# Kernel tuning notes

Measured on AMD Instinct MI355X. Metric: run time of the kernel, lower is better.

The kernel has to match this reference:

```python
import jax, jax.numpy as jnp
import numpy as np

HIDDEN = 2048
HEADS = 16
HEAD_DIM = HIDDEN // HEADS  # 128
MLA_DIM = max(HEAD_DIM // 4, 8)  # 32
WINDOW = 512
B, S = 4, 2048


def setup_inputs() -> dict:
    key = jax.random.key(0)
    ks = jax.random.split(key, 9)
    sc = 0.02
    return {
        "x": jax.random.normal(ks[0], (B, S, HIDDEN), jnp.float32),
        "wq": jax.random.normal(ks[1], (HIDDEN, HIDDEN), jnp.float32) * sc,
        "wk": jax.random.normal(ks[2], (HEAD_DIM, HIDDEN), jnp.float32) * sc,
        "wv": jax.random.normal(ks[3], (HEAD_DIM, HIDDEN), jnp.float32) * sc,
        "wo": jax.random.normal(ks[4], (HIDDEN, HIDDEN), jnp.float32) * sc,
        "k_compress_w": jax.random.normal(ks[5], (MLA_DIM, HEAD_DIM), jnp.float32) * sc,
        "v_compress_w": jax.random.normal(ks[6], (MLA_DIM, HEAD_DIM), jnp.float32) * sc,
        "k_decompress_w": jax.random.normal(ks[7], (HEAD_DIM, MLA_DIM), jnp.float32) * sc,
        "v_decompress_w": jax.random.normal(ks[8], (HEAD_DIM, MLA_DIM), jnp.float32) * sc,
    }


def _rope_tables(seq_len, dim):
    inv_freq = 1.0 / (10000.0 ** (jnp.arange(0, dim, 2, dtype=jnp.float32) / dim))
    t = jnp.arange(seq_len, dtype=jnp.float32)
    freqs = jnp.outer(t, inv_freq)            # [S, dim/2]
    emb = jnp.concatenate([freqs, freqs], -1)  # [S, dim]
    return jnp.cos(emb), jnp.sin(emb)


def _rotate_half(x):
    h = x.shape[-1] // 2
    return jnp.concatenate([-x[..., h:], x[..., :h]], axis=-1)


def _quant_dequant_8bit(t):
    # global min/max 8-bit fake-quant (round has zero grad, matching uint8 detach)
    t_min, t_max = t.min(), t.max()
    scale = (t_max - t_min) / 255.0
    q = jnp.clip(jnp.round((t - t_min) / scale), 0.0, 255.0)
    return q * scale + t_min


def _swat(scores):
    attn = jax.nn.sigmoid(scores)
    return attn / (attn.sum(axis=-1, keepdims=True) + 1e-8)


def reference(x, wq, wk, wv, wo, k_compress_w, v_compress_w, k_decompress_w, v_decompress_w):
    b, s, _ = x.shape
    scale = 1.0 / np.sqrt(HEAD_DIM)

    Q = (x @ wq.T).reshape(b, s, HEADS, HEAD_DIM).transpose(0, 2, 1, 3)  # [B,H,S,D]
    K = (x @ wk.T)[:, None]  # [B,1,S,D] (single shared KV head, MQA)
    V = (x @ wv.T)[:, None]

    # RoPE (cos/sin broadcast over batch and heads)
    cos, sin = _rope_tables(s, HEAD_DIM)
    Q = Q * cos + _rotate_half(Q) * sin
    K = K * cos + _rotate_half(K) * sin

    # MLA compress -> decompress (low-rank)
    K = (K @ k_compress_w.T) @ k_decompress_w.T
    V = (V @ v_compress_w.T) @ v_decompress_w.T

    # 8-bit fake quantization
    K = _quant_dequant_8bit(K)
    V = _quant_dequant_8bit(V)

    # Sliding-window SWAT attention with linear blending of overlaps
    step = WINDOW // 2
    out = jnp.zeros_like(Q)
    for i in range(0, s, step):
        e = min(i + WINDOW, s)
        Qw = Q[:, :, i:e]           # [B,H,w,D]
        Kw = K[:, :, i:e]           # [B,1,w,D]
        Vw = V[:, :, i:e]
        scores = jnp.matmul(Qw, Kw.swapaxes(-2, -1)) * scale  # [B,H,w,w]
        wout = jnp.matmul(_swat(scores), Vw)                   # [B,H,w,D]
        if i == 0:
            out = out.at[:, :, i:e].set(wout)
        else:
            ov = min(step, e - i)
            alpha = jnp.linspace(0.0, 1.0, ov).reshape(1, 1, -1, 1)
            blended = (1 - alpha) * out[:, :, i:i + ov] + alpha * wout[:, :, :ov]
            out = out.at[:, :, i:i + ov].set(blended)
            if i + ov < e:
                out = out.at[:, :, i + ov:e].set(wout[:, :, ov:])

    out = out.transpose(0, 2, 1, 3).reshape(b, s, HIDDEN)
    return out @ wo.T
```

## Files before the change

### kernel.cpp

```cpp
#include <hip/hip_runtime.h>
#include <hip/hip_bf16.h>
#include <hip/hip_fp16.h>
#include <math.h>

#define BB 4
#define SS 2048
#define HIDDEN 2048
#define NHEADS 16
#define HDIM 128
#define BSROWS (BB * SS)
#define ATT_SCALE 0.08838834764831845f

typedef __attribute__((ext_vector_type(8))) _Float16 half8v;
typedef __attribute__((ext_vector_type(4))) float f32x4;
typedef __attribute__((ext_vector_type(16))) float f32x16;

static __device__ __forceinline__ unsigned encf(float x) {
  unsigned b = __float_as_uint(x);
  return (b & 0x80000000u) ? ~b : (b | 0x80000000u);
}
static __device__ __forceinline__ float decf(unsigned k) {
  unsigned b = (k & 0x80000000u) ? (k ^ 0x80000000u) : ~k;
  return __uint_as_float(b);
}
static __device__ __forceinline__ unsigned short f2h(float f) {
  _Float16 h = (_Float16)f;
  return *(unsigned short*)&h;
}


__global__ void rope_tables_k(float* __restrict__ ct, float* __restrict__ st) {
  int t = blockIdx.x;
  int d = threadIdx.x;
  float inv = powf(10000.0f, -(float)d * (1.0f / 64.0f));
  float a = (float)t * inv;
  ct[t * 64 + d] = cosf(a);
  st[t * 64 + d] = sinf(a);
}

__global__ void build_m_k(const float* __restrict__ kc, const float* __restrict__ kdw,
                          const float* __restrict__ vc, const float* __restrict__ vdw,
                          float* __restrict__ mk, float* __restrict__ mv) {
  int a = blockIdx.x;
  int c = threadIdx.x;
  const float* cw = blockIdx.y ? vc : kc;
  const float* dw = blockIdx.y ? vdw : kdw;
  float* m = blockIdx.y ? mv : mk;
  float acc = 0.f;
#pragma unroll
  for (int mm = 0; mm < 32; mm++) acc += cw[mm * 128 + a] * dw[c * 32 + mm];
  m[a * 128 + c] = acc;
}

__global__ void mm_init_k(unsigned* mmx) {
  int i = threadIdx.x;
  if (i < 4) mmx[i] = (i & 1) ? 0u : 0xFFFFFFFFu;
}

__global__ void split_fp16_k(const float* __restrict__ src,
                             unsigned short* __restrict__ hi, int n4) {
  int i = blockIdx.x * 256 + threadIdx.x;
  int stride = gridDim.x * 256;
  for (; i < n4; i += stride) {
    float4 v = ((const float4*)src)[i];
    ((ushort4*)hi)[i] = make_ushort4(f2h(v.x), f2h(v.y), f2h(v.z), f2h(v.w));
  }
}

__global__ __launch_bounds__(512, 2) void gemm_f16_ph_k(
    const unsigned short* __restrict__ A, const unsigned short* __restrict__ B,
    float* __restrict__ Cf, unsigned short* __restrict__ Ch, int NBX) {
  __shared__ unsigned short As[2][256 * 64];
  __shared__ unsigned short Bs[2][256 * 64];
  const int K = 2048;
  const int nsteps = 32;
  int tid = threadIdx.x;
  int lane = tid & 63;
  int wid = tid >> 6;
  int wm = wid >> 2, wn = wid & 3;
  int l31 = lane & 31, lg2 = lane >> 5;
  int swz = (l31 & 7) << 4;

  int nwg = gridDim.x;
  int cpx = nwg >> 3;
  int sbid = ((int)blockIdx.x & 7) * cpx + ((int)blockIdx.x >> 3);
  int by = sbid / NBX, bx = sbid % NBX;
  int m0 = by * 256, n0 = bx * 256;

  f32x16 acc[4][2] = {};

#define STAGE_A_HALF(tt_, h_, sl_)                                                 \
  do {                                                                             \
    int k0a_ = (tt_) << 6;                                                         \
    _Pragma("unroll") for (int j_ = 0; j_ < 2; ++j_) {                             \
      int L_ = j_ * 8192 + tid * 16;                                               \
      int hr_ = L_ >> 7;                                                           \
      int r_ = (hr_ & 63) + ((hr_ & 64) << 1) + (h_) * 64;                         \
      int cb_ = (L_ & 127) ^ ((r_ & 7) << 4);                                      \
      __builtin_amdgcn_global_load_lds(                                            \
          (const __attribute__((address_space(1))) void*)(A +                      \
              (size_t)(m0 + r_) * K + k0a_ + (cb_ >> 1)),                          \
          (__attribute__((address_space(3))) void*)((char*)&As[sl_][0] +           \
              (h_) * 8192 + j_ * 16384 + tid * 16), 16, 0, 0);                     \
    }                                                                              \
  } while (0)

#define STAGE_B_HALF(tt_, h_, sl_)                                                 \
  do {                                                                             \
    int k0b_ = (tt_) << 6;                                                         \
    _Pragma("unroll") for (int j_ = 0; j_ < 2; ++j_) {                             \
      int L_ = j_ * 8192 + tid * 16;                                               \
      int hr_ = L_ >> 7;                                                           \
      int r_ = (hr_ & 63) + ((hr_ & 64) << 1) + (h_) * 64;                         \
      int cb_ = (L_ & 127) ^ ((r_ & 7) << 4);                                      \
      __builtin_amdgcn_global_load_lds(                                            \
          (const __attribute__((address_space(1))) void*)(B +                      \
              (size_t)(n0 + r_) * K + k0b_ + (cb_ >> 1)),                          \
          (__attribute__((address_space(3))) void*)((char*)&Bs[sl_][0] +           \
              (h_) * 8192 + j_ * 16384 + tid * 16), 16, 0, 0);                     \
    }                                                                              \
  } while (0)

  STAGE_A_HALF(0, 0, 0);
  STAGE_B_HALF(0, 0, 0);
  STAGE_B_HALF(0, 1, 0);
  STAGE_A_HALF(0, 1, 0);
  asm volatile("s_waitcnt vmcnt(0)" ::: "memory");
  __builtin_amdgcn_sched_barrier(0);
  __builtin_amdgcn_s_barrier();

  for (int t = 0; t < nsteps; ++t) {
    int s = t & 1;
    const char* Ab = (const char*)&As[s][0];
    const char* Bb = (const char*)&Bs[s][0];
    half8v afr[2][4], bfr[2][4];
    if (t + 1 < nsteps) {
      STAGE_A_HALF(t + 1, 0, s ^ 1);
      STAGE_B_HALF(t + 1, 0, s ^ 1);
      STAGE_B_HALF(t + 1, 1, s ^ 1);
      STAGE_A_HALF(t + 1, 1, s ^ 1);
    }
#pragma unroll
    for (int ks = 0; ks < 4; ++ks) {
      int cb = (ks * 32 + lg2 * 16) ^ swz;
      afr[0][ks] = *(const half8v*)(Ab + (wm * 128 + 0 + l31) * 128 + cb);
      afr[1][ks] = *(const half8v*)(Ab + (wm * 128 + 32 + l31) * 128 + cb);
      bfr[0][ks] = *(const half8v*)(Bb + (wn * 64 + 0 + l31) * 128 + cb);
      bfr[1][ks] = *(const half8v*)(Bb + (wn * 64 + 32 + l31) * 128 + cb);
    }
    __builtin_amdgcn_s_barrier();
    asm volatile("s_waitcnt lgkmcnt(0)" ::: "memory");
    __builtin_amdgcn_sched_barrier(0);
    __builtin_amdgcn_s_setprio(1);
#pragma unroll
    for (int ks = 0; ks < 4; ++ks) {
      acc[0][0] = __builtin_amdgcn_mfma_f32_32x32x16_f16(afr[0][ks], bfr[0][ks], acc[0][0], 0, 0, 0);
      acc[0][1] = __builtin_amdgcn_mfma_f32_32x32x16_f16(afr[0][ks], bfr[1][ks], acc[0][1], 0, 0, 0);
      acc[1][0] = __builtin_amdgcn_mfma_f32_32x32x16_f16(afr[1][ks], bfr[0][ks], acc[1][0], 0, 0, 0);
      acc[1][1] = __builtin_amdgcn_mfma_f32_32x32x16_f16(afr[1][ks], bfr[1][ks], acc[1][1], 0, 0, 0);
    }
    __builtin_amdgcn_s_setprio(0);
    if (t + 1 < nsteps)
      asm volatile("s_waitcnt vmcnt(8)" ::: "memory");
    else
      asm volatile("s_waitcnt vmcnt(0)" ::: "memory");
    __builtin_amdgcn_sched_barrier(0);
    __builtin_amdgcn_s_barrier();
#pragma unroll
    for (int ks = 0; ks < 4; ++ks) {
      int cb = (ks * 32 + lg2 * 16) ^ swz;
      afr[0][ks] = *(const half8v*)(Ab + (wm * 128 + 64 + l31) * 128 + cb);
      afr[1][ks] = *(const half8v*)(Ab + (wm * 128 + 96 + l31) * 128 + cb);
    }
    __builtin_amdgcn_s_barrier();
    asm volatile("s_waitcnt lgkmcnt(0)" ::: "memory");
    __builtin_amdgcn_sched_barrier(0);
    __builtin_amdgcn_s_setprio(1);
#pragma unroll
    for (int ks = 0; ks < 4; ++ks) {
      acc[2][0] = __builtin_amdgcn_mfma_f32_32x32x16_f16(afr[0][ks], bfr[0][ks], acc[2][0], 0, 0, 0);
      acc[2][1] = __builtin_amdgcn_mfma_f32_32x32x16_f16(afr[0][ks], bfr[1][ks], acc[2][1], 0, 0, 0);
      acc[3][0] = __builtin_amdgcn_mfma_f32_32x32x16_f16(afr[1][ks], bfr[0][ks], acc[3][0], 0, 0, 0);
      acc[3][1] = __builtin_amdgcn_mfma_f32_32x32x16_f16(afr[1][ks], bfr[1][ks], acc[3][1], 0, 0, 0);
    }
    __builtin_amdgcn_s_setprio(0);
    if (t + 1 < nsteps)
      asm volatile("s_waitcnt vmcnt(2)" ::: "memory");
    else
      asm volatile("s_waitcnt vmcnt(0)" ::: "memory");
    __builtin_amdgcn_sched_barrier(0);
    __builtin_amdgcn_s_barrier();
  }
#undef STAGE_A_HALF
#undef STAGE_B_HALF

#pragma unroll
  for (int mi = 0; mi < 4; ++mi) {
#pragma unroll
    for (int ni = 0; ni < 2; ++ni) {
      int col = n0 + wn * 64 + ni * 32 + l31;
#pragma unroll
      for (int r = 0; r < 16; ++r) {
        int row = m0 + wm * 128 + mi * 32 + (r & 3) + 8 * (r >> 2) + 4 * lg2;
        float v = acc[mi][ni][r];
        if (Ch)
          Ch[(size_t)row * 2048 + col] = f2h(v);
        else
          Cf[(size_t)row * 2048 + col] = v;
      }
    }
  }
}

__global__ __launch_bounds__(256) void gemm_f16_kv_k(
    const unsigned short* __restrict__ A, const unsigned short* __restrict__ B,
    float* __restrict__ Ckv) {
  const int K = 2048;
  __shared__ unsigned short As[128 * 64];
  __shared__ unsigned short Bs[128 * 64];
  int tid = threadIdx.x;
  int lane = tid & 63, wid = tid >> 6;
  int wr = wid >> 1, wc = wid & 1;
  int m0 = blockIdx.y * 128, n0 = blockIdx.x * 128;

  f32x4 acc[4][4] = {};

  int off_ = (wid << 10) + (lane << 4);
  int l15 = lane & 15, lk = lane >> 4;

  for (int t = 0; t < 32; ++t) {
    int k0 = t << 6;
    __syncthreads();
#pragma unroll
    for (int c = 0; c < 4; ++c) {
      int off = off_ + (c << 12);
      int row = off >> 7;
      int cole = (off & 127) >> 1;
      const unsigned short* ga = A + (size_t)(m0 + row) * K + k0 + cole;
      const unsigned short* gb = B + (size_t)(n0 + row) * K + k0 + cole;
      __builtin_amdgcn_global_load_lds(
          (const __attribute__((address_space(1))) void*)ga,
          (__attribute__((address_space(3))) void*)((char*)As + off), 16, 0, 0);
      __builtin_amdgcn_global_load_lds(
          (const __attribute__((address_space(1))) void*)gb,
          (__attribute__((address_space(3))) void*)((char*)Bs + off), 16, 0, 0);
    }
    __syncthreads();
#pragma unroll
    for (int ks = 0; ks < 2; ++ks) {
      half8v af[4], bf[4];
#pragma unroll
      for (int f = 0; f < 4; ++f) {
        int arow = wr * 64 + f * 16 + l15;
        int brow = wc * 64 + f * 16 + l15;
        int colb = ks * 64 + lk * 16;
        af[f] = *(const half8v*)((const char*)As + arow * 128 + colb);
        bf[f] = *(const half8v*)((const char*)Bs + brow * 128 + colb);
      }
#pragma unroll
      for (int fm = 0; fm < 4; ++fm)
#pragma unroll
        for (int fn = 0; fn < 4; ++fn)
          acc[fm][fn] = __builtin_amdgcn_mfma_f32_16x16x32_f16(af[fm], bf[fn], acc[fm][fn], 0, 0, 0);
    }
  }
#pragma unroll
  for (int fm = 0; fm < 4; ++fm) {
#pragma unroll
    for (int j = 0; j < 4; ++j) {
      int row = m0 + wr * 64 + fm * 16 + lk * 4 + j;
#pragma unroll
      for (int fn = 0; fn < 4; ++fn) {
        int col = n0 + wc * 64 + fn * 16 + l15;
        Ckv[(size_t)row * 256 + col] = acc[fm][fn][j];
      }
    }
  }
}

__global__ __launch_bounds__(256) void kv_transform_k(float* kvb,
                                                      const float* __restrict__ mk,
                                                      const float* __restrict__ mv,
                                                      const float* __restrict__ ct,
                                                      const float* __restrict__ st,
                                                      unsigned* mmx) {
  int which = blockIdx.y;
  float* base = kvb + which * 128;
  const float* M = which ? mv : mk;
  __shared__ float rowb[256];
  __shared__ float red[256];
  int tid = threadIdx.x;
  int half = tid >> 7, col = tid & 127;
  float vmin = 3.4e38f, vmax = -3.4e38f;
  int r0 = blockIdx.x * 64;
  for (int ri = 0; ri < 32; ri++) {
    size_t row = r0 + ri * 2 + half;
    __syncthreads();
    if (which == 0) {
      int t = (int)(row & (SS - 1));
      int j = col & 63;
      float c = ct[t * 64 + j], s = st[t * 64 + j];
      float x0 = base[row * 256 + j];
      float x1 = base[row * 256 + j + 64];
      rowb[tid] = (col < 64) ? (x0 * c - x1 * s) : (x1 * c + x0 * s);
    } else {
      rowb[tid] = base[row * 256 + col];
    }
    __syncthreads();
    float acc = 0.f;
    const float* rb = &rowb[half * 128];
#pragma unroll 8
    for (int a = 0; a < 128; a++) acc += rb[a] * M[a * 128 + col];
    base[row * 256 + col] = acc;
    vmin = fminf(vmin, acc);
    vmax = fmaxf(vmax, acc);
  }
  red[tid] = vmin;
  __syncthreads();
  for (int s2 = 128; s2 > 0; s2 >>= 1) {
    if (tid < s2) red[tid] = fminf(red[tid], red[tid + s2]);
    __syncthreads();
  }
  if (tid == 0) atomicMin(&mmx[which * 2 + 0], encf(red[0]));
  __syncthreads();
  red[tid] = vmax;
  __syncthreads();
  for (int s2 = 128; s2 > 0; s2 >>= 1) {
    if (tid < s2) red[tid] = fmaxf(red[tid], red[tid + s2]);
    __syncthreads();
  }
  if (tid == 0) atomicMax(&mmx[which * 2 + 1], encf(red[0]));
}

__global__ void quant_k_codes_k(const float* __restrict__ kvb,
                                unsigned short* __restrict__ qkc,
                                const unsigned* __restrict__ mmx) {
  int i = blockIdx.x * 256 + threadIdx.x;
  float mn = decf(mmx[0]);
  float sc = (decf(mmx[1]) - mn) * (1.f / 255.f);
  int row = i >> 7, d = i & 127;
  float v = kvb[(size_t)row * 256 + d];
  float qv = fminf(fmaxf(rintf((v - mn) / sc), 0.f), 255.f);
  qkc[i] = f2h(qv);
}

__global__ __launch_bounds__(256) void quant_vt_k(const float* __restrict__ kvb,
                                                  unsigned short* __restrict__ qvtc,
                                                  const unsigned* __restrict__ mmx) {
  int b = blockIdx.y;
  int s0 = blockIdx.x * 64;
  __shared__ unsigned short tile[128 * 72];
  float mn = decf(mmx[2]);
  float sc = (decf(mmx[3]) - mn) * (1.f / 255.f);
  for (int i = threadIdx.x; i < 8192; i += 256) {
    int sl = i >> 7, d = i & 127;
    float v = kvb[((size_t)(b * SS + s0 + sl)) * 256 + 128 + d];
    float qv = fminf(fmaxf(rintf((v - mn) / sc), 0.f), 255.f);
    tile[d * 72 + sl] = f2h(qv);
  }
  __syncthreads();
  int d = threadIdx.x >> 1, hf = threadIdx.x & 1;
  unsigned short* dst = qvtc + (size_t)(b * 128 + d) * 2048 + s0 + hf * 32;
  const unsigned short* srcp = &tile[d * 72 + hf * 32];
#pragma unroll
  for (int u = 0; u < 4; ++u)
    *(ushort4*)(dst + u * 8) = *(const ushort4*)(srcp + u * 8),
    *(ushort4*)(dst + u * 8 + 4) = *(const ushort4*)(srcp + u * 8 + 4);
}

__global__ __launch_bounds__(256, 3) void attn_mfma_k(
    const unsigned short* __restrict__ qh, const unsigned short* __restrict__ qkc,
    const unsigned short* __restrict__ qvtc, const unsigned* __restrict__ mmx,
    const float* __restrict__ ct, const float* __restrict__ st,
    unsigned short* __restrict__ outp) {
  __shared__ unsigned short Ks[64 * 128];
  __shared__ unsigned short Vt[128 * 64];
  __shared__ unsigned short Pl[64 * 64];
  int tid = threadIdx.x;
  int lane = tid & 63, w = tid >> 6;
  int l15 = lane & 15, lg = lane >> 4;
  int swk = (l15 & 7) << 4;
  int b = blockIdx.y >> 4, h = blockIdx.y & 15;
  int t0 = blockIdx.x * 64;
  int wa = t0 >> 8;

  float mnk = decf(mmx[0]), sck = (decf(mmx[1]) - mnk) * (1.f / 255.f);
  float mnv = decf(mmx[2]), scv = (decf(mmx[3]) - mnv) * (1.f / 255.f);
  float aK = ATT_SCALE * sck;
  float aMnk = ATT_SCALE * mnk;

  half8v qf[4];
  float cj[4];
  {
    int trow = t0 + w * 16 + l15;
    const unsigned short* qrow =
        qh + ((size_t)(b * SS + trow) * NHEADS + h) * HDIM + lg * 8;
    const float* cbp = ct + (size_t)trow * 64 + lg * 8;
    const float* sbp = st + (size_t)trow * 64 + lg * 8;
    float sq = 0.f;
#pragma unroll
    for (int half = 0; half < 2; ++half) {
      half8v xa8 = *(const half8v*)(qrow + half * 32);
      half8v ya8 = *(const half8v*)(qrow + half * 32 + 64);
      float4 ca = *(const float4*)(cbp + half * 32);
      float4 cb4 = *(const float4*)(cbp + half * 32 + 4);
      float4 sa = *(const float4*)(sbp + half * 32);
      float4 sb4 = *(const float4*)(sbp + half * 32 + 4);
      float cv[8] = {ca.x, ca.y, ca.z, ca.w, cb4.x, cb4.y, cb4.z, cb4.w};
      float sv[8] = {sa.x, sa.y, sa.z, sa.w, sb4.x, sb4.y, sb4.z, sb4.w};
      half8v tlo, thi;
#pragma unroll
      for (int u = 0; u < 8; ++u) {
        float xv = (float)xa8[u], yv = (float)ya8[u];
        float r0 = xv * cv[u] - yv * sv[u];
        float r1 = yv * cv[u] + xv * sv[u];
        sq += r0 + r1;
        tlo[u] = (_Float16)r0;
        thi[u] = (_Float16)r1;
      }
      qf[half] = tlo;
      qf[half + 2] = thi;
      __builtin_amdgcn_sched_barrier(0);
    }
    sq += __shfl_xor(sq, 16);
    sq += __shfl_xor(sq, 32);
#pragma unroll
    for (int j = 0; j < 4; ++j) cj[j] = aMnk * __shfl(sq, lg * 4 + j);
  }

  f32x4 zz = {0.f, 0.f, 0.f, 0.f};
  f32x4 acc0[8], acc1[8];
#pragma unroll
  for (int i = 0; i < 8; ++i) { acc0[i] = zz; acc1[i] = zz; }
  float rs0[4] = {0, 0, 0, 0}, rs1[4] = {0, 0, 0, 0};
  int base = wa * 256;

  int n = (wa == 0 || wa == 7) ? 8 : 12;
  int segoff = (wa == 0) ? 1 : 0;
  int kbase = (wa == 0) ? base : base - 256;

#define STAGE_K(K0)                                                                \
  do {                                                                             \
    int k0_ = (K0);                                                                \
    const char* kb_ = (const char*)qkc + ((size_t)b * SS + k0_) * 256;             \
    _Pragma("unroll") for (int i_ = 0; i_ < 4; ++i_) {                             \
      int L_ = w * 4096 + i_ * 1024 + lane * 16;                                   \
      int kr_ = L_ >> 8;                                                           \
      int kd_ = (L_ & 255) ^ ((kr_ & 7) << 4);                                     \
      __builtin_amdgcn_global_load_lds(                                            \
          (const __attribute__((address_space(1))) void*)(kb_ + kr_ * 256 + kd_),  \
          (__attribute__((address_space(3))) void*)((char*)Ks + L_), 16, 0, 0);    \
    }                                                                              \
  } while (0)

#define STAGE_V(K0)                                                                \
  do {                                                                             \
    int k0_ = (K0);                                                                \
    const char* vb_ = (const char*)qvtc + (size_t)b * 524288 + (size_t)k0_ * 2;    \
    _Pragma("unroll") for (int i_ = 0; i_ < 4; ++i_) {                             \
      int L_ = w * 4096 + i_ * 1024 + lane * 16;                                   \
      int vr_ = L_ >> 7;                                                           \
      int vd_ = (L_ & 127) ^ ((vr_ & 7) << 4);                                     \
      __builtin_amdgcn_global_load_lds(                                            \
          (const __attribute__((address_space(1))) void*)(vb_ + vr_ * 4096 + vd_), \
          (__attribute__((address_space(3))) void*)((char*)Vt + L_), 16, 0, 0);    \
    }                                                                              \
  } while (0)

  STAGE_K(kbase);
  STAGE_V(kbase);
  asm volatile("s_waitcnt vmcnt(4)" ::: "memory");
  __builtin_amdgcn_sched_barrier(0);
  __builtin_amdgcn_s_barrier();

  for (int i = 0; i < n; ++i) {
    int sg = segoff + (i >> 2);
    bool d0 = (sg <= 1) && (wa > 0);
    bool d1 = (sg >= 1);
    {
      f32x4 sf0 = zz, sf1 = zz, sf2 = zz, sf3 = zz;
#pragma unroll
      for (int kk = 0; kk < 4; ++kk) {
        int cb = (kk * 64 + lg * 16) ^ swk;
        half8v k0f = *(const half8v*)((const char*)Ks + (0 * 16 + l15) * 256 + cb);
        half8v k1f = *(const half8v*)((const char*)Ks + (1 * 16 + l15) * 256 + cb);
        half8v k2f = *(const half8v*)((const char*)Ks + (2 * 16 + l15) * 256 + cb);
        half8v k3f = *(const half8v*)((const char*)Ks + (3 * 16 + l15) * 256 + cb);
        sf0 = __builtin_amdgcn_mfma_f32_16x16x32_f16(qf[kk], k0f, sf0, 0, 0, 0);
        sf1 = __builtin_amdgcn_mfma_f32_16x16x32_f16(qf[kk], k1f, sf1, 0, 0, 0);
        sf2 = __builtin_amdgcn_mfma_f32_16x16x32_f16(qf[kk], k2f, sf2, 0, 0, 0);
        sf3 = __builtin_amdgcn_mfma_f32_16x16x32_f16(qf[kk], k3f, sf3, 0, 0, 0);
      }
      float rsc[4] = {0.f, 0.f, 0.f, 0.f};
#pragma unroll
      for (int nf = 0; nf < 4; ++nf) {
        f32x4 sv = (nf == 0) ? sf0 : (nf == 1) ? sf1 : (nf == 2) ? sf2 : sf3;
#pragma unroll
        for (int j = 0; j < 4; ++j) {
          float s_ = aK * sv[j] + cj[j];
          float p_ = 1.f / (1.f + __expf(-s_));
          rsc[j] += p_;
          int prow = w * 16 + lg * 4 + j;
          int paddr = prow * 128 + (((nf * 16 + l15) * 2) ^ ((prow & 7) << 4));
          *(unsigned short*)((char*)Pl + paddr) = f2h(p_);
        }
      }
#pragma unroll
      for (int j = 0; j < 4; ++j) {
        rsc[j] += __shfl_xor(rsc[j], 1);
        rsc[j] += __shfl_xor(rsc[j], 2);
        rsc[j] += __shfl_xor(rsc[j], 4);
        rsc[j] += __shfl_xor(rsc[j], 8);
        if (d0) rs0[j] += rsc[j];
        if (d1) rs1[j] += rsc[j];
      }
    }
    __builtin_amdgcn_s_barrier();
    if (i + 1 < n) {
      STAGE_K(kbase + (i + 1) * 64);
      asm volatile("s_waitcnt vmcnt(4)" ::: "memory");
    } else {
      asm volatile("s_waitcnt vmcnt(0)" ::: "memory");
    }
    __builtin_amdgcn_sched_barrier(0);
    __builtin_amdgcn_s_barrier();
    {
      half8v pf0, pf1;
      int prow = w * 16 + l15;
      pf0 = *(const half8v*)((const char*)Pl + prow * 128 + ((lg * 16) ^ swk));
      pf1 = *(const half8v*)((const char*)Pl + prow * 128 + ((64 + lg * 16) ^ swk));
#pragma unroll
      for (int nf = 0; nf < 8; ++nf) {
        int vb0 = (nf * 16 + l15) * 128 + ((lg * 16) ^ swk);
        int vb1 = (nf * 16 + l15) * 128 + ((64 + lg * 16) ^ swk);
        half8v vf0 = *(const half8v*)((const char*)Vt + vb0);
        half8v vf1 = *(const half8v*)((const char*)Vt + vb1);
        if (d0) {
          acc0[nf] = __builtin_amdgcn_mfma_f32_16x16x32_f16(pf0, vf0, acc0[nf], 0, 0, 0);
          acc0[nf] = __builtin_amdgcn_mfma_f32_16x16x32_f16(pf1, vf1, acc0[nf], 0, 0, 0);
        }
        if (d1) {
          acc1[nf] = __builtin_amdgcn_mfma_f32_16x16x32_f16(pf0, vf0, acc1[nf], 0, 0, 0);
          acc1[nf] = __builtin_amdgcn_mfma_f32_16x16x32_f16(pf1, vf1, acc1[nf], 0, 0, 0);
        }
      }
    }
    __builtin_amdgcn_s_barrier();
    if (i + 1 < n) {
      STAGE_V(kbase + (i + 1) * 64);
      asm volatile("s_waitcnt vmcnt(4)" ::: "memory");
      __builtin_amdgcn_sched_barrier(0);
      __builtin_amdgcn_s_barrier();
    }
  }
#undef STAGE_K
#undef STAGE_V

#pragma unroll
  for (int j = 0; j < 4; ++j) {
    int t = t0 + w * 16 + lg * 4 + j;
    float al = (float)(t & 255) * (1.f / 255.f);
    float r0 = rs0[j], r1 = rs1[j];
    float i0 = 1.f / (r0 + 1e-8f), i1 = 1.f / (r1 + 1e-8f);
    float w0 = (wa == 0) ? 0.f : (1.f - al);
    float w1 = (wa == 0) ? 1.f : al;
    size_t obase = ((size_t)(b * SS + t) * NHEADS + h) * HDIM;
#pragma unroll
    for (int nf = 0; nf < 8; ++nf) {
      float o0 = (scv * acc0[nf][j] + mnv * r0) * i0;
      float o1 = (scv * acc1[nf][j] + mnv * r1) * i1;
      outp[obase + nf * 16 + l15] = f2h(w0 * o0 + w1 * o1);
    }
  }
}

extern "C" void kernel_launch(void* const* d_in, const int* in_sizes, int n_in,
                              void* d_out, int out_size, void* d_ws, size_t ws_size,
                              hipStream_t stream) {
  const float* x = (const float*)d_in[0];
  const float* wq = (const float*)d_in[1];
  const float* wk = (const float*)d_in[2];
  const float* wv = (const float*)d_in[3];
  const float* wo = (const float*)d_in[4];
  const float* kcw = (const float*)d_in[5];
  const float* vcw = (const float*)d_in[6];
  const float* kdw = (const float*)d_in[7];
  const float* vdw = (const float*)d_in[8];
  float* out = (float*)d_out;

  const size_t QN = (size_t)BSROWS * HIDDEN;
  const size_t KVN = (size_t)BSROWS * 256;

  unsigned short* qh = (unsigned short*)d_ws;
  float* kvb = (float*)(qh + QN);
  float* ct = kvb + KVN;
  float* st = ct + SS * 64;
  float* mk = st + SS * 64;
  float* mv = mk + 128 * 128;
  unsigned* mmx = (unsigned*)(mv + 128 * 128);
  unsigned short* xh = (unsigned short*)(mmx + 16);
  unsigned short* wqkvh = xh + QN;
  unsigned short* woh = wqkvh + (size_t)2304 * 2048;
  unsigned short* qkc = woh + (size_t)HIDDEN * HIDDEN;
  unsigned short* qvtc = qkc + (size_t)BSROWS * 128;

  rope_tables_k<<<SS, 64, 0, stream>>>(ct, st);
  build_m_k<<<dim3(128, 2), 128, 0, stream>>>(kcw, kdw, vcw, vdw, mk, mv);

  split_fp16_k<<<2048, 256, 0, stream>>>(x, xh, (int)(QN / 4));
  split_fp16_k<<<512, 256, 0, stream>>>(wq, wqkvh, HIDDEN * HIDDEN / 4);
  split_fp16_k<<<256, 256, 0, stream>>>(wk, wqkvh + (size_t)2048 * 2048, HDIM * HIDDEN / 4);
  split_fp16_k<<<256, 256, 0, stream>>>(wv, wqkvh + (size_t)2176 * 2048, HDIM * HIDDEN / 4);
  split_fp16_k<<<512, 256, 0, stream>>>(wo, woh, HIDDEN * HIDDEN / 4);

  gemm_f16_kv_k<<<dim3(2, 64), 256, 0, stream>>>(xh, wqkvh + (size_t)2048 * 2048, kvb);
  gemm_f16_ph_k<<<256, 512, 0, stream>>>(xh, wqkvh, nullptr, qh, 8);

  mm_init_k<<<1, 64, 0, stream>>>(mmx);
  kv_transform_k<<<dim3(BSROWS / 64, 2), 256, 0, stream>>>(kvb, mk, mv, ct, st, mmx);
  quant_k_codes_k<<<(BSROWS * 128) / 256, 256, 0, stream>>>(kvb, qkc, mmx);
  quant_vt_k<<<dim3(SS / 64, BB), 256, 0, stream>>>(kvb, qvtc, mmx);

  attn_mfma_k<<<dim3(SS / 64, BB * NHEADS), 256, 0, stream>>>(qh, qkc, qvtc, mmx, ct, st,
                                                              xh);

  gemm_f16_ph_k<<<256, 512, 0, stream>>>(xh, woh, out, nullptr, 8);
}
```

Measured before the change: 554.6 us.

## Split attention PV output dims across paired waves with 512-thread blocks

The attention block grows from 4 to 8 waves. Even waves compute QK^T scores and the sigmoid probabilities, and each wave pair splits the 128 output dims of the PV product into two halves, so per-wave accumulators are halved. K/V staging is spread over all 512 threads, and row sums are shared through LDS before the final blend. This is meant to cut per-wave register pressure and raise PV parallelism, but odd waves sit idle during the score phase and the launch bounds change alters the occupancy trade-off.

```diff
diff --git a/kernel.cpp b/kernel.cpp
--- a/kernel.cpp
+++ b/kernel.cpp
@@ -368,7 +368,7 @@
     *(ushort4*)(dst + u * 8 + 4) = *(const ushort4*)(srcp + u * 8 + 4);
 }
 
-__global__ __launch_bounds__(256, 3) void attn_mfma_k(
+__global__ __launch_bounds__(512) void attn_mfma_k(
     const unsigned short* __restrict__ qh, const unsigned short* __restrict__ qkc,
     const unsigned short* __restrict__ qvtc, const unsigned* __restrict__ mmx,
     const float* __restrict__ ct, const float* __restrict__ st,
@@ -378,6 +378,7 @@
   __shared__ unsigned short Pl[64 * 64];
   int tid = threadIdx.x;
   int lane = tid & 63, w = tid >> 6;
+  int p = w >> 1, ohalf = w & 1;
   int l15 = lane & 15, lg = lane >> 4;
   int swk = (l15 & 7) << 4;
   int b = blockIdx.y >> 4, h = blockIdx.y & 15;
@@ -391,8 +392,8 @@
 
   half8v qf[4];
   float cj[4];
-  {
-    int trow = t0 + w * 16 + l15;
+  if ((w & 1) == 0) {
+    int trow = t0 + p * 16 + l15;
     const unsigned short* qrow =
         qh + ((size_t)(b * SS + trow) * NHEADS + h) * HDIM + lg * 8;
     const float* cbp = ct + (size_t)trow * 64 + lg * 8;
@@ -429,9 +430,9 @@
   }
 
   f32x4 zz = {0.f, 0.f, 0.f, 0.f};
-  f32x4 acc0[8], acc1[8];
-#pragma unroll
-  for (int i = 0; i < 8; ++i) { acc0[i] = zz; acc1[i] = zz; }
+  f32x4 acc0[4], acc1[4];
+#pragma unroll
+  for (int i = 0; i < 4; ++i) { acc0[i] = zz; acc1[i] = zz; }
   float rs0[4] = {0, 0, 0, 0}, rs1[4] = {0, 0, 0, 0};
   int base = wa * 256;
 
@@ -443,8 +444,8 @@
   do {                                                                             \
     int k0_ = (K0);                                                                \
     const char* kb_ = (const char*)qkc + ((size_t)b * SS + k0_) * 256;             \
-    _Pragma("unroll") for (int i_ = 0; i_ < 4; ++i_) {                             \
-      int L_ = w * 4096 + i_ * 1024 + lane * 16;                                   \
+    _Pragma("unroll") for (int i_ = 0; i_ < 2; ++i_) {                             \
+      int L_ = i_ * 8192 + tid * 16;                                               \
       int kr_ = L_ >> 8;                                                           \
       int kd_ = (L_ & 255) ^ ((kr_ & 7) << 4);                                     \
       __builtin_amdgcn_global_load_lds(                                            \
@@ -457,8 +458,8 @@
   do {                                                                             \
     int k0_ = (K0);                                                                \
     const char* vb_ = (const char*)qvtc + (size_t)b * 524288 + (size_t)k0_ * 2;    \
-    _Pragma("unroll") for (int i_ = 0; i_ < 4; ++i_) {                             \
-      int L_ = w * 4096 + i_ * 1024 + lane * 16;                                   \
+    _Pragma("unroll") for (int i_ = 0; i_ < 2; ++i_) {                             \
+      int L_ = i_ * 8192 + tid * 16;                                               \
       int vr_ = L_ >> 7;                                                           \
       int vd_ = (L_ & 127) ^ ((vr_ & 7) << 4);                                     \
       __builtin_amdgcn_global_load_lds(                                            \
@@ -469,7 +470,7 @@
 
   STAGE_K(kbase);
   STAGE_V(kbase);
-  asm volatile("s_waitcnt vmcnt(4)" ::: "memory");
+  asm volatile("s_waitcnt vmcnt(2)" ::: "memory");
   __builtin_amdgcn_sched_barrier(0);
   __builtin_amdgcn_s_barrier();
 
@@ -477,7 +478,7 @@
     int sg = segoff + (i >> 2);
     bool d0 = (sg <= 1) && (wa > 0);
     bool d1 = (sg >= 1);
-    {
+    if ((w & 1) == 0) {
       f32x4 sf0 = zz, sf1 = zz, sf2 = zz, sf3 = zz;
 #pragma unroll
       for (int kk = 0; kk < 4; ++kk) {
@@ -500,7 +501,7 @@
           float s_ = aK * sv[j] + cj[j];
           float p_ = 1.f / (1.f + __expf(-s_));
           rsc[j] += p_;
-          int prow = w * 16 + lg * 4 + j;
+          int prow = p * 16 + lg * 4 + j;
           int paddr = prow * 128 + (((nf * 16 + l15) * 2) ^ ((prow & 7) << 4));
           *(unsigned short*)((char*)Pl + paddr) = f2h(p_);
         }
@@ -518,7 +519,7 @@
     __builtin_amdgcn_s_barrier();
     if (i + 1 < n) {
       STAGE_K(kbase + (i + 1) * 64);
-      asm volatile("s_waitcnt vmcnt(4)" ::: "memory");
+      asm volatile("s_waitcnt vmcnt(2)" ::: "memory");
     } else {
       asm volatile("s_waitcnt vmcnt(0)" ::: "memory");
     }
@@ -526,13 +527,14 @@
     __builtin_amdgcn_s_barrier();
     {
       half8v pf0, pf1;
-      int prow = w * 16 + l15;
+      int prow = p * 16 + l15;
       pf0 = *(const half8v*)((const char*)Pl + prow * 128 + ((lg * 16) ^ swk));
       pf1 = *(const half8v*)((const char*)Pl + prow * 128 + ((64 + lg * 16) ^ swk));
 #pragma unroll
-      for (int nf = 0; nf < 8; ++nf) {
-        int vb0 = (nf * 16 + l15) * 128 + ((lg * 16) ^ swk);
-        int vb1 = (nf * 16 + l15) * 128 + ((64 + lg * 16) ^ swk);
+      for (int nf = 0; nf < 4; ++nf) {
+        int dim = ohalf * 64 + nf * 16 + l15;
+        int vb0 = dim * 128 + ((lg * 16) ^ swk);
+        int vb1 = dim * 128 + ((64 + lg * 16) ^ swk);
         half8v vf0 = *(const half8v*)((const char*)Vt + vb0);
         half8v vf1 = *(const half8v*)((const char*)Vt + vb1);
         if (d0) {
@@ -548,7 +550,7 @@
     __builtin_amdgcn_s_barrier();
     if (i + 1 < n) {
       STAGE_V(kbase + (i + 1) * 64);
-      asm volatile("s_waitcnt vmcnt(4)" ::: "memory");
+      asm volatile("s_waitcnt vmcnt(2)" ::: "memory");
       __builtin_amdgcn_sched_barrier(0);
       __builtin_amdgcn_s_barrier();
     }
@@ -556,20 +558,31 @@
 #undef STAGE_K
 #undef STAGE_V
 
+  float* rsl = (float*)Ks;
+  if ((w & 1) == 0 && l15 == 0) {
+#pragma unroll
+    for (int j = 0; j < 4; ++j) {
+      rsl[p * 16 + lg * 4 + j] = rs0[j];
+      rsl[64 + p * 16 + lg * 4 + j] = rs1[j];
+    }
+  }
+  __syncthreads();
+
 #pragma unroll
   for (int j = 0; j < 4; ++j) {
-    int t = t0 + w * 16 + lg * 4 + j;
+    int row = p * 16 + lg * 4 + j;
+    int t = t0 + row;
     float al = (float)(t & 255) * (1.f / 255.f);
-    float r0 = rs0[j], r1 = rs1[j];
+    float r0 = rsl[row], r1 = rsl[64 + row];
     float i0 = 1.f / (r0 + 1e-8f), i1 = 1.f / (r1 + 1e-8f);
     float w0 = (wa == 0) ? 0.f : (1.f - al);
     float w1 = (wa == 0) ? 1.f : al;
     size_t obase = ((size_t)(b * SS + t) * NHEADS + h) * HDIM;
 #pragma unroll
-    for (int nf = 0; nf < 8; ++nf) {
+    for (int nf = 0; nf < 4; ++nf) {
       float o0 = (scv * acc0[nf][j] + mnv * r0) * i0;
       float o1 = (scv * acc1[nf][j] + mnv * r1) * i1;
-      outp[obase + nf * 16 + l15] = f2h(w0 * o0 + w1 * o1);
+      outp[obase + ohalf * 64 + nf * 16 + l15] = f2h(w0 * o0 + w1 * o1);
     }
   }
 }
@@ -621,7 +634,7 @@
   quant_k_codes_k<<<(BSROWS * 128) / 256, 256, 0, stream>>>(kvb, qkc, mmx);
   quant_vt_k<<<dim3(SS / 64, BB), 256, 0, stream>>>(kvb, qvtc, mmx);
 
-  attn_mfma_k<<<dim3(SS / 64, BB * NHEADS), 256, 0, stream>>>(qh, qkc, qvtc, mmx, ct, st,
+  attn_mfma_k<<<dim3(SS / 64, BB * NHEADS), 512, 0, stream>>>(qh, qkc, qvtc, mmx, ct, st,
                                                               xh);
 
   gemm_f16_ph_k<<<256, 512, 0, stream>>>(xh, woh, out, nullptr, 8);
```

After: 651.3 us. +17.4%, slower.
